# Performance work log

Hardware: AMD Instinct MI355X
Metric: run time of the kernel (lower is better)

The kernel has to match this reference:

```python
import jax, jax.numpy as jnp
import numpy as np

B, H, I = 64, 4096, 14336   # batch, hidden, expert intermediate
NLUT = 4096                 # 2**L_bits, L=12
W_SCALE = 0.02              # payload['W_scale'] (same for all three here)


def _rademacher(key, shape):
    return jnp.where(jax.random.bernoulli(key, 0.5, shape), 1.0, -1.0).astype(jnp.float32)


def setup_inputs() -> dict:
    key = jax.random.key(0)
    ks = jax.random.split(key, 14)
    inp = {
        "x": jax.random.normal(ks[0], (B, H), jnp.float32),
        "lut_gate": jax.random.normal(ks[1], (NLUT,), jnp.float32) * 0.05,
        "lut_up": jax.random.normal(ks[2], (NLUT,), jnp.float32) * 0.05,
        "lut_down": jax.random.normal(ks[3], (NLUT,), jnp.float32) * 0.05,
        "gate_walks": jax.random.randint(ks[4], (I, H), 0, NLUT, jnp.int32),
        "up_walks": jax.random.randint(ks[5], (I, H), 0, NLUT, jnp.int32),
        "down_walks": jax.random.randint(ks[6], (H, I), 0, NLUT, jnp.int32),
        "gate_sign_l": _rademacher(ks[7], (I,)),
        "gate_sign_r": _rademacher(ks[8], (H,)),
        "up_sign_l": _rademacher(ks[9], (I,)),
        "up_sign_r": _rademacher(ks[10], (H,)),
        "down_sign_l": _rademacher(ks[11], (H,)),
        "down_sign_r": _rademacher(ks[12], (I,)),
    }
    return inp


def _dequant(lut, walks, sign_l, sign_r):
    # trellis-walk LUT gather per weight element, then row/col signs and scalar scale
    # walks: (out, in) int codes; lut: (NLUT,)
    return (lut[walks] * sign_l[:, None] * sign_r[None, :]) * W_SCALE


def reference(x, lut_gate, lut_up, lut_down,
              gate_walks, up_walks, down_walks,
              gate_sign_l, gate_sign_r, up_sign_l, up_sign_r,
              down_sign_l, down_sign_r):
    W_gate = _dequant(lut_gate, gate_walks, gate_sign_l, gate_sign_r)  # (I, H)
    W_up = _dequant(lut_up, up_walks, up_sign_l, up_sign_r)            # (I, H)
    W_down = _dequant(lut_down, down_walks, down_sign_l, down_sign_r)  # (H, I)
    gate_out = jax.nn.silu(x @ W_gate.T)   # (B, I)
    up_out = x @ W_up.T                    # (B, I)
    hidden = gate_out * up_out
    return hidden @ W_down.T               # (B, H)
```

## Files before the change

kernel.cpp:

```cpp
#include <hip/hip_runtime.h>
#include <hip/hip_bf16.h>

#define HD   4096
#define ID   14336
#define NB   64
#define NLUTN 4096
#define KSPLIT 4

typedef __attribute__((ext_vector_type(8))) short short8;
typedef __attribute__((ext_vector_type(4))) float f32x4;

__device__ __forceinline__ unsigned short f2bf(float f) {
  __hip_bfloat16 h = __float2bfloat16(f);
  return __builtin_bit_cast(unsigned short, h);
}

__global__ __launch_bounds__(256) void prep_kernel(
    const float* __restrict__ x, const float* __restrict__ gsr,
    const float* __restrict__ usr,
    unsigned short* __restrict__ xg, unsigned short* __restrict__ xu)
{
  int t = blockIdx.x * 256 + threadIdx.x;
  float4 xv = ((const float4*)x)[t];
  int hs = t & (HD/4 - 1);
  float4 g = ((const float4*)gsr)[hs];
  float4 u = ((const float4*)usr)[hs];
  ushort4 og = make_ushort4(f2bf(xv.x*g.x), f2bf(xv.y*g.y), f2bf(xv.z*g.z), f2bf(xv.w*g.w));
  ushort4 ou = make_ushort4(f2bf(xv.x*u.x), f2bf(xv.y*u.y), f2bf(xv.z*u.z), f2bf(xv.w*u.w));
  ((ushort4*)xg)[t] = og;
  ((ushort4*)xu)[t] = ou;
}

__global__ __launch_bounds__(256, 4) void gate_up_kernel(
    const int* __restrict__ gw, const int* __restrict__ uw,
    const float* __restrict__ lutg_f, const float* __restrict__ lutu_f,
    const unsigned short* __restrict__ xg, const unsigned short* __restrict__ xu,
    const float* __restrict__ gsl, const float* __restrict__ usl,
    const float* __restrict__ dsr,
    unsigned short* __restrict__ hidden)
{
  __shared__ unsigned short lutg[NLUTN];
  __shared__ unsigned short lutu[NLUTN];
  __shared__ f32x4 red[3][8][64];

  const int tid  = threadIdx.x;
  const int lane = tid & 63;
  const int w    = tid >> 6;

  #pragma unroll
  for (int i = tid; i < NLUTN/4; i += 256) {
    float4 g = ((const float4*)lutg_f)[i];
    float4 u = ((const float4*)lutu_f)[i];
    ((ushort4*)lutg)[i] = make_ushort4(f2bf(g.x), f2bf(g.y), f2bf(g.z), f2bf(g.w));
    ((ushort4*)lutu)[i] = make_ushort4(f2bf(u.x), f2bf(u.y), f2bf(u.z), f2bf(u.w));
  }
  __syncthreads();

  const int col  = lane & 15;
  const int quad = lane >> 4;
  const int m0   = blockIdx.x * 16;

  const int kbeg = w * (HD / 4);
  const int kend = kbeg + (HD / 4);

  const int* gp = gw + (size_t)(m0 + col) * HD + quad * 8;
  const int* up = uw + (size_t)(m0 + col) * HD + quad * 8;
  const unsigned short* xgp[4];
  const unsigned short* xup[4];
  #pragma unroll
  for (int t = 0; t < 4; ++t) {
    xgp[t] = xg + (size_t)(t*16 + col) * HD + quad * 8;
    xup[t] = xu + (size_t)(t*16 + col) * HD + quad * 8;
  }

  const f32x4 z = {0.f, 0.f, 0.f, 0.f};
  f32x4 accg[4] = {z, z, z, z};
  f32x4 accu[4] = {z, z, z, z};

  int4 cga = *(const int4*)(gp + kbeg);
  int4 cgb = *(const int4*)(gp + kbeg + 4);
  int4 cua = *(const int4*)(up + kbeg);
  int4 cub = *(const int4*)(up + kbeg + 4);

  for (int k0 = kbeg; k0 < kend; k0 += 32) {
    int kn = k0 + 32;
    if (kn >= kend) kn = kbeg;
    int4 nga = *(const int4*)(gp + kn);
    int4 ngb = *(const int4*)(gp + kn + 4);
    int4 nua = *(const int4*)(up + kn);
    int4 nub = *(const int4*)(up + kn + 4);

    short8 afg, afu;
    afg[0] = (short)lutg[cga.x]; afg[1] = (short)lutg[cga.y];
    afg[2] = (short)lutg[cga.z]; afg[3] = (short)lutg[cga.w];
    afg[4] = (short)lutg[cgb.x]; afg[5] = (short)lutg[cgb.y];
    afg[6] = (short)lutg[cgb.z]; afg[7] = (short)lutg[cgb.w];
    afu[0] = (short)lutu[cua.x]; afu[1] = (short)lutu[cua.y];
    afu[2] = (short)lutu[cua.z]; afu[3] = (short)lutu[cua.w];
    afu[4] = (short)lutu[cub.x]; afu[5] = (short)lutu[cub.y];
    afu[6] = (short)lutu[cub.z]; afu[7] = (short)lutu[cub.w];

    #pragma unroll
    for (int t = 0; t < 4; ++t) {
      short8 bg = __builtin_bit_cast(short8, *(const int4*)(xgp[t] + k0));
      short8 bu = __builtin_bit_cast(short8, *(const int4*)(xup[t] + k0));
      accg[t] = __builtin_amdgcn_mfma_f32_16x16x32_bf16(afg, bg, accg[t], 0, 0, 0);
      accu[t] = __builtin_amdgcn_mfma_f32_16x16x32_bf16(afu, bu, accu[t], 0, 0, 0);
    }

    cga = nga; cgb = ngb; cua = nua; cub = nub;
  }

  if (w > 0) {
    #pragma unroll
    for (int t = 0; t < 4; ++t) {
      red[w-1][t][lane]     = accg[t];
      red[w-1][4 + t][lane] = accu[t];
    }
  }
  __syncthreads();
  if (w == 0) {
    #pragma unroll
    for (int ww = 0; ww < 3; ++ww) {
      #pragma unroll
      for (int t = 0; t < 4; ++t) {
        accg[t] += red[ww][t][lane];
        accu[t] += red[ww][4 + t][lane];
      }
    }

    const int mrow = m0 + quad * 4;
    float sg[4], su[4], sd[4];
    #pragma unroll
    for (int r = 0; r < 4; ++r) {
      sg[r] = 0.02f * gsl[mrow + r];
      su[r] = 0.02f * usl[mrow + r];
      sd[r] = dsr[mrow + r];
    }
    #pragma unroll
    for (int t = 0; t < 4; ++t) {
      int b = t*16 + col;
      ushort4 hv;
      float g0 = accg[t][0] * sg[0], u0 = accu[t][0] * su[0];
      float g1 = accg[t][1] * sg[1], u1 = accu[t][1] * su[1];
      float g2 = accg[t][2] * sg[2], u2 = accu[t][2] * su[2];
      float g3 = accg[t][3] * sg[3], u3 = accu[t][3] * su[3];
      hv.x = f2bf((g0 / (1.f + __expf(-g0))) * u0 * sd[0]);
      hv.y = f2bf((g1 / (1.f + __expf(-g1))) * u1 * sd[1]);
      hv.z = f2bf((g2 / (1.f + __expf(-g2))) * u2 * sd[2]);
      hv.w = f2bf((g3 / (1.f + __expf(-g3))) * u3 * sd[3]);
      *((ushort4*)(hidden + (size_t)b * ID + mrow)) = hv;
    }
  }
}

__global__ __launch_bounds__(256, 4) void down_kernel(
    const int* __restrict__ dw, const float* __restrict__ lutd_f,
    const unsigned short* __restrict__ hidden,
    const float* __restrict__ dsl,
    float* __restrict__ out)
{
  __shared__ unsigned short lutd[NLUTN];
  __shared__ f32x4 red[3][4][64];

  const int tid  = threadIdx.x;
  const int lane = tid & 63;
  const int w    = tid >> 6;

  #pragma unroll
  for (int i = tid; i < NLUTN/4; i += 256) {
    float4 d = ((const float4*)lutd_f)[i];
    ((ushort4*)lutd)[i] = make_ushort4(f2bf(d.x), f2bf(d.y), f2bf(d.z), f2bf(d.w));
  }
  __syncthreads();

  const int col  = lane & 15;
  const int quad = lane >> 4;
  const int m0   = blockIdx.x * 16;
  const int kchunk = ID / KSPLIT;
  const int kbeg = blockIdx.y * kchunk + w * (kchunk / 4);
  const int kend = kbeg + kchunk / 4;

  const int* dp = dw + (size_t)(m0 + col) * ID + quad * 8;
  const unsigned short* hp[4];
  #pragma unroll
  for (int t = 0; t < 4; ++t)
    hp[t] = hidden + (size_t)(t*16 + col) * ID + quad * 8;

  const f32x4 z = {0.f, 0.f, 0.f, 0.f};
  f32x4 acc[4] = {z, z, z, z};

  int4 cda = *(const int4*)(dp + kbeg);
  int4 cdb = *(const int4*)(dp + kbeg + 4);

  for (int k0 = kbeg; k0 < kend; k0 += 32) {
    int kn = k0 + 32;
    if (kn >= kend) kn = kbeg;
    int4 nda = *(const int4*)(dp + kn);
    int4 ndb = *(const int4*)(dp + kn + 4);

    short8 af;
    af[0] = (short)lutd[cda.x]; af[1] = (short)lutd[cda.y];
    af[2] = (short)lutd[cda.z]; af[3] = (short)lutd[cda.w];
    af[4] = (short)lutd[cdb.x]; af[5] = (short)lutd[cdb.y];
    af[6] = (short)lutd[cdb.z]; af[7] = (short)lutd[cdb.w];

    #pragma unroll
    for (int t = 0; t < 4; ++t) {
      short8 bh = __builtin_bit_cast(short8, *(const int4*)(hp[t] + k0));
      acc[t] = __builtin_amdgcn_mfma_f32_16x16x32_bf16(af, bh, acc[t], 0, 0, 0);
    }

    cda = nda; cdb = ndb;
  }

  if (w > 0) {
    #pragma unroll
    for (int t = 0; t < 4; ++t) red[w-1][t][lane] = acc[t];
  }
  __syncthreads();
  if (w == 0) {
    #pragma unroll
    for (int ww = 0; ww < 3; ++ww) {
      #pragma unroll
      for (int t = 0; t < 4; ++t) acc[t] += red[ww][t][lane];
    }

    const int mrow = m0 + quad * 4;
    float sc[4];
    #pragma unroll
    for (int r = 0; r < 4; ++r) sc[r] = 0.02f * dsl[mrow + r];
    #pragma unroll
    for (int t = 0; t < 4; ++t) {
      int b = t*16 + col;
      #pragma unroll
      for (int r = 0; r < 4; ++r)
        atomicAdd(&out[(size_t)b * HD + mrow + r], acc[t][r] * sc[r]);
    }
  }
}

extern "C" void kernel_launch(void* const* d_in, const int* in_sizes, int n_in,
                              void* d_out, int out_size, void* d_ws, size_t ws_size,
                              hipStream_t stream) {
  const float* x    = (const float*)d_in[0];
  const float* lutg = (const float*)d_in[1];
  const float* lutu = (const float*)d_in[2];
  const float* lutd = (const float*)d_in[3];
  const int*   gw   = (const int*)d_in[4];
  const int*   uw   = (const int*)d_in[5];
  const int*   dw   = (const int*)d_in[6];
  const float* gsl  = (const float*)d_in[7];
  const float* gsr  = (const float*)d_in[8];
  const float* usl  = (const float*)d_in[9];
  const float* usr  = (const float*)d_in[10];
  const float* dsl  = (const float*)d_in[11];
  const float* dsr  = (const float*)d_in[12];
  float* out = (float*)d_out;

  unsigned short* xg     = (unsigned short*)d_ws;
  unsigned short* xu     = xg + (size_t)NB * HD;
  unsigned short* hidden = xu + (size_t)NB * HD;

  hipMemsetAsync(d_out, 0, (size_t)NB * HD * sizeof(float), stream);
  prep_kernel<<<(NB*HD/4 + 255)/256, 256, 0, stream>>>(x, gsr, usr, xg, xu);
  gate_up_kernel<<<ID/16, 256, 0, stream>>>(gw, uw, lutg, lutu, xg, xu,
                                            gsl, usl, dsr, hidden);
  down_kernel<<<dim3(HD/16, KSPLIT), 256, 0, stream>>>(dw, lutd, hidden, dsl, out);
}
```

Before: 758.7 us.

## Stage walk codes via global_load_lds double buffer, 32-row tiles, blocked activation layout

Both GEMM kernels now stream the int32 walk codes into swizzled LDS double buffers with global_load_lds, instead of per-lane register prefetch. Each wave covers 32 output rows, which doubles reuse of the activation fragments, using 2 waves per block instead of 4. The activations and hidden tensors are stored in a k8-blocked layout so each MFMA B-fragment is one contiguous 16-byte load. The down projection uses a split-K of 8 to keep the grid large. The cost is fewer waves per block, a full vmcnt(0) wait each iteration, and more LDS per block.

Measured after the change: 655.5 us. 1.16x faster.

```diff
diff --git a/kernel.cpp b/kernel.cpp
--- a/kernel.cpp
+++ b/kernel.cpp
@@ -5,7 +5,7 @@
 #define ID   14336
 #define NB   64
 #define NLUTN 4096
-#define KSPLIT 4
+#define DKS  8
 
 typedef __attribute__((ext_vector_type(8))) short short8;
 typedef __attribute__((ext_vector_type(4))) float f32x4;
@@ -15,40 +15,54 @@
   return __builtin_bit_cast(unsigned short, h);
 }
 
+__device__ __forceinline__ void gll16(const int* g, void* l) {
+  __builtin_amdgcn_global_load_lds(
+      (const __attribute__((address_space(1))) int*)g,
+      (__attribute__((address_space(3))) int*)l, 16, 0, 0);
+}
+
 __global__ __launch_bounds__(256) void prep_kernel(
     const float* __restrict__ x, const float* __restrict__ gsr,
     const float* __restrict__ usr,
-    unsigned short* __restrict__ xg, unsigned short* __restrict__ xu)
+    unsigned short* __restrict__ xgB, unsigned short* __restrict__ xuB)
 {
-  int t = blockIdx.x * 256 + threadIdx.x;
-  float4 xv = ((const float4*)x)[t];
-  int hs = t & (HD/4 - 1);
-  float4 g = ((const float4*)gsr)[hs];
-  float4 u = ((const float4*)usr)[hs];
-  ushort4 og = make_ushort4(f2bf(xv.x*g.x), f2bf(xv.y*g.y), f2bf(xv.z*g.z), f2bf(xv.w*g.w));
-  ushort4 ou = make_ushort4(f2bf(xv.x*u.x), f2bf(xv.y*u.y), f2bf(xv.z*u.z), f2bf(xv.w*u.w));
-  ((ushort4*)xg)[t] = og;
-  ((ushort4*)xu)[t] = ou;
-}
-
-__global__ __launch_bounds__(256, 4) void gate_up_kernel(
+  int u = blockIdx.x * 256 + threadIdx.x;
+  int b = u & 63, k8 = u >> 6;
+  const float* xp = x + (size_t)b * HD + k8 * 8;
+  float4 x0 = ((const float4*)xp)[0];
+  float4 x1 = ((const float4*)xp)[1];
+  const float* gp = gsr + k8 * 8;
+  const float* up = usr + k8 * 8;
+  float4 g0 = ((const float4*)gp)[0], g1 = ((const float4*)gp)[1];
+  float4 u0 = ((const float4*)up)[0], u1 = ((const float4*)up)[1];
+  ushort4 og0 = make_ushort4(f2bf(x0.x*g0.x), f2bf(x0.y*g0.y), f2bf(x0.z*g0.z), f2bf(x0.w*g0.w));
+  ushort4 og1 = make_ushort4(f2bf(x1.x*g1.x), f2bf(x1.y*g1.y), f2bf(x1.z*g1.z), f2bf(x1.w*g1.w));
+  ushort4 ou0 = make_ushort4(f2bf(x0.x*u0.x), f2bf(x0.y*u0.y), f2bf(x0.z*u0.z), f2bf(x0.w*u0.w));
+  ushort4 ou1 = make_ushort4(f2bf(x1.x*u1.x), f2bf(x1.y*u1.y), f2bf(x1.z*u1.z), f2bf(x1.w*u1.w));
+  ((ushort4*)(xgB + (size_t)u*8))[0] = og0;
+  ((ushort4*)(xgB + (size_t)u*8))[1] = og1;
+  ((ushort4*)(xuB + (size_t)u*8))[0] = ou0;
+  ((ushort4*)(xuB + (size_t)u*8))[1] = ou1;
+}
+
+__global__ __launch_bounds__(128, 2) void gate_up_kernel(
     const int* __restrict__ gw, const int* __restrict__ uw,
     const float* __restrict__ lutg_f, const float* __restrict__ lutu_f,
-    const unsigned short* __restrict__ xg, const unsigned short* __restrict__ xu,
+    const unsigned short* __restrict__ xgB, const unsigned short* __restrict__ xuB,
     const float* __restrict__ gsl, const float* __restrict__ usl,
     const float* __restrict__ dsr,
-    unsigned short* __restrict__ hidden)
+    unsigned short* __restrict__ hidB)
 {
   __shared__ unsigned short lutg[NLUTN];
   __shared__ unsigned short lutu[NLUTN];
-  __shared__ f32x4 red[3][8][64];
+  __shared__ __align__(16) int cbuf[2][2][2][2][512];
+  __shared__ f32x4 red[16][64];
 
   const int tid  = threadIdx.x;
   const int lane = tid & 63;
   const int w    = tid >> 6;
 
-  #pragma unroll
-  for (int i = tid; i < NLUTN/4; i += 256) {
+  for (int i = tid; i < NLUTN/4; i += 128) {
     float4 g = ((const float4*)lutg_f)[i];
     float4 u = ((const float4*)lutu_f)[i];
     ((ushort4*)lutg)[i] = make_ushort4(f2bf(g.x), f2bf(g.y), f2bf(g.z), f2bf(g.w));
@@ -58,117 +72,147 @@
 
   const int col  = lane & 15;
   const int quad = lane >> 4;
-  const int m0   = blockIdx.x * 16;
-
-  const int kbeg = w * (HD / 4);
-  const int kend = kbeg + (HD / 4);
-
-  const int* gp = gw + (size_t)(m0 + col) * HD + quad * 8;
-  const int* up = uw + (size_t)(m0 + col) * HD + quad * 8;
-  const unsigned short* xgp[4];
-  const unsigned short* xup[4];
+  const int m0   = blockIdx.x * 32;
+  const int r8   = lane >> 3;
+  const int j    = lane & 7;
+  const int jx   = (j ^ r8) << 2;
+  const int xsw  = (col & 7) << 4;
+
+  const int kbeg = w * (HD/2);
+  const int NIT  = (HD/2) / 32;
+
+  const int* gsrc[2][2];
+  const int* usrc[2][2];
   #pragma unroll
-  for (int t = 0; t < 4; ++t) {
-    xgp[t] = xg + (size_t)(t*16 + col) * HD + quad * 8;
-    xup[t] = xu + (size_t)(t*16 + col) * HD + quad * 8;
-  }
+  for (int s = 0; s < 2; ++s)
+    #pragma unroll
+    for (int h = 0; h < 2; ++h) {
+      int row = m0 + s*16 + h*8 + r8;
+      gsrc[s][h] = gw + (size_t)row * HD + jx;
+      usrc[s][h] = uw + (size_t)row * HD + jx;
+    }
 
   const f32x4 z = {0.f, 0.f, 0.f, 0.f};
-  f32x4 accg[4] = {z, z, z, z};
-  f32x4 accu[4] = {z, z, z, z};
-
-  int4 cga = *(const int4*)(gp + kbeg);
-  int4 cgb = *(const int4*)(gp + kbeg + 4);
-  int4 cua = *(const int4*)(up + kbeg);
-  int4 cub = *(const int4*)(up + kbeg + 4);
-
-  for (int k0 = kbeg; k0 < kend; k0 += 32) {
-    int kn = k0 + 32;
-    if (kn >= kend) kn = kbeg;
-    int4 nga = *(const int4*)(gp + kn);
-    int4 ngb = *(const int4*)(gp + kn + 4);
-    int4 nua = *(const int4*)(up + kn);
-    int4 nub = *(const int4*)(up + kn + 4);
-
-    short8 afg, afu;
-    afg[0] = (short)lutg[cga.x]; afg[1] = (short)lutg[cga.y];
-    afg[2] = (short)lutg[cga.z]; afg[3] = (short)lutg[cga.w];
-    afg[4] = (short)lutg[cgb.x]; afg[5] = (short)lutg[cgb.y];
-    afg[6] = (short)lutg[cgb.z]; afg[7] = (short)lutg[cgb.w];
-    afu[0] = (short)lutu[cua.x]; afu[1] = (short)lutu[cua.y];
-    afu[2] = (short)lutu[cua.z]; afu[3] = (short)lutu[cua.w];
-    afu[4] = (short)lutu[cub.x]; afu[5] = (short)lutu[cub.y];
-    afu[6] = (short)lutu[cub.z]; afu[7] = (short)lutu[cub.w];
-
+  f32x4 accg[2][4] = {{z,z,z,z},{z,z,z,z}};
+  f32x4 accu[2][4] = {{z,z,z,z},{z,z,z,z}};
+
+  #pragma unroll
+  for (int s = 0; s < 2; ++s)
+    #pragma unroll
+    for (int h = 0; h < 2; ++h) {
+      gll16(gsrc[s][h] + kbeg, (char*)&cbuf[w][0][0][s][0] + h*1024);
+      gll16(usrc[s][h] + kbeg, (char*)&cbuf[w][0][1][s][0] + h*1024);
+    }
+
+  int p = 0;
+  for (int it = 0; it < NIT; ++it) {
+    const int k0 = kbeg + it*32;
+    asm volatile("s_waitcnt vmcnt(0)" ::: "memory");
+    __builtin_amdgcn_sched_barrier(0);
+
+    short8 afg[2], afu[2];
+    #pragma unroll
+    for (int s = 0; s < 2; ++s) {
+      const char* cg = (const char*)&cbuf[w][p][0][s][0];
+      const char* cu = (const char*)&cbuf[w][p][1][s][0];
+      int4 ga = *(const int4*)(cg + col*128 + (((quad<<5) + 0 ) ^ xsw));
+      int4 gb = *(const int4*)(cg + col*128 + (((quad<<5) + 16) ^ xsw));
+      int4 ua = *(const int4*)(cu + col*128 + (((quad<<5) + 0 ) ^ xsw));
+      int4 ub = *(const int4*)(cu + col*128 + (((quad<<5) + 16) ^ xsw));
+      afg[s][0] = (short)lutg[ga.x]; afg[s][1] = (short)lutg[ga.y];
+      afg[s][2] = (short)lutg[ga.z]; afg[s][3] = (short)lutg[ga.w];
+      afg[s][4] = (short)lutg[gb.x]; afg[s][5] = (short)lutg[gb.y];
+      afg[s][6] = (short)lutg[gb.z]; afg[s][7] = (short)lutg[gb.w];
+      afu[s][0] = (short)lutu[ua.x]; afu[s][1] = (short)lutu[ua.y];
+      afu[s][2] = (short)lutu[ua.z]; afu[s][3] = (short)lutu[ua.w];
+      afu[s][4] = (short)lutu[ub.x]; afu[s][5] = (short)lutu[ub.y];
+      afu[s][6] = (short)lutu[ub.z]; afu[s][7] = (short)lutu[ub.w];
+    }
+
+    const size_t xoff = ((size_t)((k0 >> 3) + quad) * 64 + col) * 8;
+    short8 bgv[4], buv[4];
     #pragma unroll
     for (int t = 0; t < 4; ++t) {
-      short8 bg = __builtin_bit_cast(short8, *(const int4*)(xgp[t] + k0));
-      short8 bu = __builtin_bit_cast(short8, *(const int4*)(xup[t] + k0));
-      accg[t] = __builtin_amdgcn_mfma_f32_16x16x32_bf16(afg, bg, accg[t], 0, 0, 0);
-      accu[t] = __builtin_amdgcn_mfma_f32_16x16x32_bf16(afu, bu, accu[t], 0, 0, 0);
-    }
-
-    cga = nga; cgb = ngb; cua = nua; cub = nub;
-  }
-
-  if (w > 0) {
-    #pragma unroll
-    for (int t = 0; t < 4; ++t) {
-      red[w-1][t][lane]     = accg[t];
-      red[w-1][4 + t][lane] = accu[t];
-    }
+      bgv[t] = __builtin_bit_cast(short8, *(const int4*)(xgB + xoff + t*128));
+      buv[t] = __builtin_bit_cast(short8, *(const int4*)(xuB + xoff + t*128));
+    }
+    __builtin_amdgcn_sched_barrier(0);
+
+    const int kn = (it == NIT-1) ? kbeg : k0 + 32;
+    #pragma unroll
+    for (int s = 0; s < 2; ++s)
+      #pragma unroll
+      for (int h = 0; h < 2; ++h) {
+        gll16(gsrc[s][h] + kn, (char*)&cbuf[w][p^1][0][s][0] + h*1024);
+        gll16(usrc[s][h] + kn, (char*)&cbuf[w][p^1][1][s][0] + h*1024);
+      }
+
+    #pragma unroll
+    for (int t = 0; t < 4; ++t)
+      #pragma unroll
+      for (int s = 0; s < 2; ++s) {
+        accg[s][t] = __builtin_amdgcn_mfma_f32_16x16x32_bf16(afg[s], bgv[t], accg[s][t], 0, 0, 0);
+        accu[s][t] = __builtin_amdgcn_mfma_f32_16x16x32_bf16(afu[s], buv[t], accu[s][t], 0, 0, 0);
+      }
+    p ^= 1;
+  }
+
+  if (w == 1) {
+    #pragma unroll
+    for (int s = 0; s < 2; ++s)
+      #pragma unroll
+      for (int t = 0; t < 4; ++t) {
+        red[(s*4+t)*2+0][lane] = accg[s][t];
+        red[(s*4+t)*2+1][lane] = accu[s][t];
+      }
   }
   __syncthreads();
   if (w == 0) {
     #pragma unroll
-    for (int ww = 0; ww < 3; ++ww) {
+    for (int s = 0; s < 2; ++s) {
+      const int mrow = m0 + s*16 + quad*4;
+      float sg[4], su[4], sd[4];
+      #pragma unroll
+      for (int r = 0; r < 4; ++r) {
+        sg[r] = 0.02f * gsl[mrow + r];
+        su[r] = 0.02f * usl[mrow + r];
+        sd[r] = dsr[mrow + r];
+      }
       #pragma unroll
       for (int t = 0; t < 4; ++t) {
-        accg[t] += red[ww][t][lane];
-        accu[t] += red[ww][4 + t][lane];
-      }
-    }
-
-    const int mrow = m0 + quad * 4;
-    float sg[4], su[4], sd[4];
-    #pragma unroll
-    for (int r = 0; r < 4; ++r) {
-      sg[r] = 0.02f * gsl[mrow + r];
-      su[r] = 0.02f * usl[mrow + r];
-      sd[r] = dsr[mrow + r];
-    }
-    #pragma unroll
-    for (int t = 0; t < 4; ++t) {
-      int b = t*16 + col;
-      ushort4 hv;
-      float g0 = accg[t][0] * sg[0], u0 = accu[t][0] * su[0];
-      float g1 = accg[t][1] * sg[1], u1 = accu[t][1] * su[1];
-      float g2 = accg[t][2] * sg[2], u2 = accu[t][2] * su[2];
-      float g3 = accg[t][3] * sg[3], u3 = accu[t][3] * su[3];
-      hv.x = f2bf((g0 / (1.f + __expf(-g0))) * u0 * sd[0]);
-      hv.y = f2bf((g1 / (1.f + __expf(-g1))) * u1 * sd[1]);
-      hv.z = f2bf((g2 / (1.f + __expf(-g2))) * u2 * sd[2]);
-      hv.w = f2bf((g3 / (1.f + __expf(-g3))) * u3 * sd[3]);
-      *((ushort4*)(hidden + (size_t)b * ID + mrow)) = hv;
-    }
-  }
-}
-
-__global__ __launch_bounds__(256, 4) void down_kernel(
+        f32x4 ag = accg[s][t] + red[(s*4+t)*2+0][lane];
+        f32x4 au = accu[s][t] + red[(s*4+t)*2+1][lane];
+        int b = t*16 + col;
+        float g0 = ag[0]*sg[0], u0 = au[0]*su[0];
+        float g1 = ag[1]*sg[1], u1 = au[1]*su[1];
+        float g2 = ag[2]*sg[2], u2 = au[2]*su[2];
+        float g3 = ag[3]*sg[3], u3 = au[3]*su[3];
+        ushort4 hv;
+        hv.x = f2bf((g0 / (1.f + __expf(-g0))) * u0 * sd[0]);
+        hv.y = f2bf((g1 / (1.f + __expf(-g1))) * u1 * sd[1]);
+        hv.z = f2bf((g2 / (1.f + __expf(-g2))) * u2 * sd[2]);
+        hv.w = f2bf((g3 / (1.f + __expf(-g3))) * u3 * sd[3]);
+        *(ushort4*)(hidB + ((size_t)((mrow >> 3)*64 + b))*8 + (quad & 1)*4) = hv;
+      }
+    }
+  }
+}
+
+__global__ __launch_bounds__(128, 2) void down_kernel(
     const int* __restrict__ dw, const float* __restrict__ lutd_f,
-    const unsigned short* __restrict__ hidden,
+    const unsigned short* __restrict__ hidB,
     const float* __restrict__ dsl,
     float* __restrict__ out)
 {
   __shared__ unsigned short lutd[NLUTN];
-  __shared__ f32x4 red[3][4][64];
+  __shared__ __align__(16) int cbuf[2][2][2][512];
+  __shared__ f32x4 red[8][64];
 
   const int tid  = threadIdx.x;
   const int lane = tid & 63;
   const int w    = tid >> 6;
 
-  #pragma unroll
-  for (int i = tid; i < NLUTN/4; i += 256) {
+  for (int i = tid; i < NLUTN/4; i += 128) {
     float4 d = ((const float4*)lutd_f)[i];
     ((ushort4*)lutd)[i] = make_ushort4(f2bf(d.x), f2bf(d.y), f2bf(d.z), f2bf(d.w));
   }
@@ -176,66 +220,96 @@
 
   const int col  = lane & 15;
   const int quad = lane >> 4;
-  const int m0   = blockIdx.x * 16;
-  const int kchunk = ID / KSPLIT;
-  const int kbeg = blockIdx.y * kchunk + w * (kchunk / 4);
-  const int kend = kbeg + kchunk / 4;
-
-  const int* dp = dw + (size_t)(m0 + col) * ID + quad * 8;
-  const unsigned short* hp[4];
+  const int m0   = blockIdx.x * 32;
+  const int r8   = lane >> 3;
+  const int j    = lane & 7;
+  const int jx   = (j ^ r8) << 2;
+  const int xsw  = (col & 7) << 4;
+
+  const int kbeg = blockIdx.y * (ID/DKS) + w * (ID/DKS/2);
+  const int NIT  = (ID/DKS/2) / 32;
+
+  const int* dsrc[2][2];
   #pragma unroll
-  for (int t = 0; t < 4; ++t)
-    hp[t] = hidden + (size_t)(t*16 + col) * ID + quad * 8;
+  for (int s = 0; s < 2; ++s)
+    #pragma unroll
+    for (int h = 0; h < 2; ++h) {
+      int row = m0 + s*16 + h*8 + r8;
+      dsrc[s][h] = dw + (size_t)row * ID + jx;
+    }
 
   const f32x4 z = {0.f, 0.f, 0.f, 0.f};
-  f32x4 acc[4] = {z, z, z, z};
-
-  int4 cda = *(const int4*)(dp + kbeg);
-  int4 cdb = *(const int4*)(dp + kbeg + 4);
-
-  for (int k0 = kbeg; k0 < kend; k0 += 32) {
-    int kn = k0 + 32;
-    if (kn >= kend) kn = kbeg;
-    int4 nda = *(const int4*)(dp + kn);
-    int4 ndb = *(const int4*)(dp + kn + 4);
-
-    short8 af;
-    af[0] = (short)lutd[cda.x]; af[1] = (short)lutd[cda.y];
-    af[2] = (short)lutd[cda.z]; af[3] = (short)lutd[cda.w];
-    af[4] = (short)lutd[cdb.x]; af[5] = (short)lutd[cdb.y];
-    af[6] = (short)lutd[cdb.z]; af[7] = (short)lutd[cdb.w];
-
-    #pragma unroll
-    for (int t = 0; t < 4; ++t) {
-      short8 bh = __builtin_bit_cast(short8, *(const int4*)(hp[t] + k0));
-      acc[t] = __builtin_amdgcn_mfma_f32_16x16x32_bf16(af, bh, acc[t], 0, 0, 0);
-    }
-
-    cda = nda; cdb = ndb;
-  }
-
-  if (w > 0) {
-    #pragma unroll
-    for (int t = 0; t < 4; ++t) red[w-1][t][lane] = acc[t];
+  f32x4 acc[2][4] = {{z,z,z,z},{z,z,z,z}};
+
+  #pragma unroll
+  for (int s = 0; s < 2; ++s)
+    #pragma unroll
+    for (int h = 0; h < 2; ++h)
+      gll16(dsrc[s][h] + kbeg, (char*)&cbuf[w][0][s][0] + h*1024);
+
+  int p = 0;
+  for (int it = 0; it < NIT; ++it) {
+    const int k0 = kbeg + it*32;
+    asm volatile("s_waitcnt vmcnt(0)" ::: "memory");
+    __builtin_amdgcn_sched_barrier(0);
+
+    short8 af[2];
+    #pragma unroll
+    for (int s = 0; s < 2; ++s) {
+      const char* cd = (const char*)&cbuf[w][p][s][0];
+      int4 da = *(const int4*)(cd + col*128 + (((quad<<5) + 0 ) ^ xsw));
+      int4 db = *(const int4*)(cd + col*128 + (((quad<<5) + 16) ^ xsw));
+      af[s][0] = (short)lutd[da.x]; af[s][1] = (short)lutd[da.y];
+      af[s][2] = (short)lutd[da.z]; af[s][3] = (short)lutd[da.w];
+      af[s][4] = (short)lutd[db.x]; af[s][5] = (short)lutd[db.y];
+      af[s][6] = (short)lutd[db.z]; af[s][7] = (short)lutd[db.w];
+    }
+
+    const size_t xoff = ((size_t)((k0 >> 3) + quad) * 64 + col) * 8;
+    short8 bh[4];
+    #pragma unroll
+    for (int t = 0; t < 4; ++t)
+      bh[t] = __builtin_bit_cast(short8, *(const int4*)(hidB + xoff + t*128));
+    __builtin_amdgcn_sched_barrier(0);
+
+    const int kn = (it == NIT-1) ? kbeg : k0 + 32;
+    #pragma unroll
+    for (int s = 0; s < 2; ++s)
+      #pragma unroll
+      for (int h = 0; h < 2; ++h)
+        gll16(dsrc[s][h] + kn, (char*)&cbuf[w][p^1][s][0] + h*1024);
+
+    #pragma unroll
+    for (int t = 0; t < 4; ++t)
+      #pragma unroll
+      for (int s = 0; s < 2; ++s)
+        acc[s][t] = __builtin_amdgcn_mfma_f32_16x16x32_bf16(af[s], bh[t], acc[s][t], 0, 0, 0);
+    p ^= 1;
+  }
+
+  if (w == 1) {
+    #pragma unroll
+    for (int s = 0; s < 2; ++s)
+      #pragma unroll
+      for (int t = 0; t < 4; ++t)
+        red[s*4+t][lane] = acc[s][t];
   }
   __syncthreads();
   if (w == 0) {
     #pragma unroll
-    for (int ww = 0; ww < 3; ++ww) {
-      #pragma unroll
-      for (int t = 0; t < 4; ++t) acc[t] += red[ww][t][lane];
-    }
-
-    const int mrow = m0 + quad * 4;
-    float sc[4];
-    #pragma unroll
-    for (int r = 0; r < 4; ++r) sc[r] = 0.02f * dsl[mrow + r];
-    #pragma unroll
-    for (int t = 0; t < 4; ++t) {
-      int b = t*16 + col;
-      #pragma unroll
-      for (int r = 0; r < 4; ++r)
-        atomicAdd(&out[(size_t)b * HD + mrow + r], acc[t][r] * sc[r]);
+    for (int s = 0; s < 2; ++s) {
+      const int mrow = m0 + s*16 + quad*4;
+      float sc[4];
+      #pragma unroll
+      for (int r = 0; r < 4; ++r) sc[r] = 0.02f * dsl[mrow + r];
+      #pragma unroll
+      for (int t = 0; t < 4; ++t) {
+        f32x4 a = acc[s][t] + red[s*4+t][lane];
+        int b = t*16 + col;
+        #pragma unroll
+        for (int r = 0; r < 4; ++r)
+          atomicAdd(&out[(size_t)b * HD + mrow + r], a[r] * sc[r]);
+      }
     }
   }
 }
@@ -258,13 +332,13 @@
   const float* dsr  = (const float*)d_in[12];
   float* out = (float*)d_out;
 
-  unsigned short* xg     = (unsigned short*)d_ws;
-  unsigned short* xu     = xg + (size_t)NB * HD;
-  unsigned short* hidden = xu + (size_t)NB * HD;
+  unsigned short* xgB  = (unsigned short*)d_ws;
+  unsigned short* xuB  = xgB + (size_t)NB * HD;
+  unsigned short* hidB = xuB + (size_t)NB * HD;
 
   hipMemsetAsync(d_out, 0, (size_t)NB * HD * sizeof(float), stream);
-  prep_kernel<<<(NB*HD/4 + 255)/256, 256, 0, stream>>>(x, gsr, usr, xg, xu);
-  gate_up_kernel<<<ID/16, 256, 0, stream>>>(gw, uw, lutg, lutu, xg, xu,
-                                            gsl, usl, dsr, hidden);
-  down_kernel<<<dim3(HD/16, KSPLIT), 256, 0, stream>>>(dw, lutd, hidden, dsl, out);
-}
+  prep_kernel<<<(NB*HD/8 + 255)/256, 256, 0, stream>>>(x, gsr, usr, xgB, xuB);
+  gate_up_kernel<<<ID/32, 128, 0, stream>>>(gw, uw, lutg, lutu, xgB, xuB,
+                                            gsl, usl, dsr, hidB);
+  down_kernel<<<dim3(HD/32, DKS), 128, 0, stream>>>(dw, lutd, hidB, dsl, out);
+}
```
